# Kernel optimization log

Hardware: AMD Instinct MI355X
Metric: run time of the kernel (lower is better)

## Reference

```python
import jax, jax.numpy as jnp
import numpy as np

N_LAYERS = 6
D_MODEL = 272          # num_variables
D_STATE = 64           # d_state
D_INNER = 2 * D_MODEL  # expand=2 -> 544
D_CONV = 4
DT_RANK = 17           # ceil(272/16)
N_SCORES = 4
B, L = 4, 2048


def setup_inputs():
    key = jax.random.key(0)
    ks = jax.random.split(key, 10)
    def rn(k, shape, s=0.02):
        return jax.random.normal(k, shape, dtype=jnp.float32) * s
    A_init = jnp.broadcast_to(jnp.arange(1, D_STATE + 1, dtype=jnp.float32), (N_LAYERS, D_INNER, D_STATE))
    return {
        "x": jax.random.normal(ks[0], (B, L, D_MODEL), dtype=jnp.float32),
        "ln_w": jnp.ones((N_LAYERS, D_MODEL), jnp.float32),
        "ln_b": jnp.zeros((N_LAYERS, D_MODEL), jnp.float32),
        "in_proj_w": rn(ks[1], (N_LAYERS, 2 * D_INNER, D_MODEL)),
        "conv_w": rn(ks[2], (N_LAYERS, D_INNER, D_CONV), 0.2),
        "conv_b": jnp.zeros((N_LAYERS, D_INNER), jnp.float32),
        "x_proj_w": rn(ks[3], (N_LAYERS, DT_RANK + 2 * D_STATE, D_INNER)),
        "dt_proj_w": rn(ks[4], (N_LAYERS, D_INNER, DT_RANK), 0.1),
        "dt_proj_b": rn(ks[5], (N_LAYERS, D_INNER), 0.5),
        "A_log": jnp.log(A_init),
        "Dskip": jnp.ones((N_LAYERS, D_INNER), jnp.float32),
        "out_proj_w": rn(ks[6], (N_LAYERS, D_MODEL, D_INNER)),
        "reg_w": rn(ks[7], (N_SCORES, D_MODEL)),
        "reg_b": jnp.zeros((N_SCORES,), jnp.float32),
    }


def _layernorm(x, w, b, eps=1e-5):
    mu = x.mean(-1, keepdims=True)
    var = ((x - mu) ** 2).mean(-1, keepdims=True)
    return (x - mu) * jax.lax.rsqrt(var + eps) * w + b


def _selective_scan(u, delta, A, Bm, C, Dd):
    # u, delta: (b,l,d); Bm, C: (b,l,n); A: (d,n); Dd: (d,)
    def step(h, inp):
        d_t, B_t, C_t, u_t = inp                           # (b,d),(b,n),(b,n),(b,d)
        dA = jnp.exp(d_t[:, :, None] * A)                  # (b,d,n)
        h = dA * h + (d_t * u_t)[:, :, None] * B_t[:, None, :]
        return h, jnp.einsum('bdn,bn->bd', h, C_t)
    h0 = jnp.zeros((u.shape[0], A.shape[0], A.shape[1]), u.dtype)
    xs = tuple(jnp.swapaxes(a, 0, 1) for a in (delta, Bm, C, u))  # time-major
    _, ys = jax.lax.scan(step, h0, xs)
    return jnp.swapaxes(ys, 0, 1) + u * Dd


def _mamba_block(x, ln_w, ln_b, Wi, cw, cb, Wx, Wdt, bdt, A_log, Dd, Wo):
    h = _layernorm(x, ln_w, ln_b)
    xi, z = jnp.split(h @ Wi.T, 2, axis=-1)                # (b,l,d_inner) each
    xp = jnp.pad(xi, ((0, 0), (D_CONV - 1, 0), (0, 0)))    # causal depthwise conv
    xc = sum(xp[:, k:k + xi.shape[1], :] * cw[:, k] for k in range(D_CONV)) + cb
    xc = jax.nn.silu(xc)
    dbl = xc @ Wx.T                                        # (b,l,dt_rank+2n)
    dt, Bm, C = jnp.split(dbl, [DT_RANK, DT_RANK + D_STATE], axis=-1)
    delta = jax.nn.softplus(dt @ Wdt.T + bdt)
    y = _selective_scan(xc, delta, -jnp.exp(A_log), Bm, C, Dd)
    y = y * jax.nn.silu(z)
    return x + y @ Wo.T                                    # residual


def reference(x, ln_w, ln_b, in_proj_w, conv_w, conv_b, x_proj_w, dt_proj_w, dt_proj_b, A_log, Dskip, out_proj_w, reg_w, reg_b):
    for i in range(N_LAYERS):
        x = _mamba_block(x, ln_w[i], ln_b[i], in_proj_w[i], conv_w[i], conv_b[i],
                         x_proj_w[i], dt_proj_w[i], dt_proj_b[i], A_log[i], Dskip[i], out_proj_w[i])
    feat = x.mean(axis=1)                                  # (b, d_model)
    scores = feat @ reg_w.T + reg_b                        # (b, n_scores)
    return (scores, feat)
```

## Files before the change

kernel.cpp:

```cpp
#include <hip/hip_runtime.h>
#include <hip/hip_bf16.h>
#include <math.h>

#define NL 6
#define DM 272
#define DS 64
#define DI 544
#define DTR 17
#define NSC 4
#define BB 4
#define LL 2048
#define MTOK (BB*LL)
#define TCH 128
#define CH  16
#define DQ  (DI/4)

typedef __attribute__((ext_vector_type(8))) short bf16x8;
typedef __attribute__((ext_vector_type(4))) float f32x4;

__device__ __forceinline__ float sigmoidf_(float x){ return 1.0f/(1.0f+__expf(-x)); }
__device__ __forceinline__ unsigned short f2bfu(float x){
    union { __hip_bfloat16 h; unsigned short u; } c; c.h = __float2bfloat16(x); return c.u;
}
__device__ __forceinline__ float exp2x(float x){ float r; asm("v_exp_f32 %0, %1" : "=v"(r) : "v"(x)); return r; }

#define DPPADD(x, ctrl) x += __int_as_float(__builtin_amdgcn_update_dpp(0, __float_as_int(x), ctrl, 0xf, 0xf, true))
__device__ __forceinline__ float wsum64(float x){
    DPPADD(x, 0x111); DPPADD(x, 0x112); DPPADD(x, 0x114); DPPADD(x, 0x118);
    DPPADD(x, 0x142); DPPADD(x, 0x143);
    return x;
}

__global__ __launch_bounds__(256) void ln_kernel(const float* __restrict__ X,
                          const float* __restrict__ w,
                          const float* __restrict__ b,
                          unsigned short* __restrict__ Hb)
{
    int wave = threadIdx.x >> 6;
    int lane = threadIdx.x & 63;
    int tok = blockIdx.x*4 + wave;
    const float* xr = X + (size_t)tok*DM;
    float v[5];
    float s=0.f, ss=0.f;
    #pragma unroll
    for (int j=0;j<5;++j){
        int idx = lane + j*64;
        float x = (idx < DM) ? xr[idx] : 0.f;
        v[j]=x; s+=x; ss+=x*x;
    }
    #pragma unroll
    for (int off=1; off<64; off<<=1){ s += __shfl_xor(s,off); ss += __shfl_xor(ss,off); }
    float mu  = s * (1.0f/DM);
    float var = ss*(1.0f/DM) - mu*mu;
    float inv = 1.0f/sqrtf(var + 1e-5f);
    unsigned short* hr = Hb + (size_t)tok*DM;
    #pragma unroll
    for (int j=0;j<5;++j){
        int idx = lane + j*64;
        if (idx<DM) hr[idx] = f2bfu((v[j]-mu)*inv*w[idx] + b[idx]);
    }
}

template<bool RESID>
__global__ __launch_bounds__(256) void gmfma(const unsigned short* __restrict__ A, int lda,
                     const unsigned short* __restrict__ W, int ldw,
                     float* __restrict__ C, int ldc,
                     const float* __restrict__ R, int ldr,
                     int N, int K)
{
    __shared__ unsigned short As[128*40];
    __shared__ unsigned short Bs[128*40];
    int bm = blockIdx.x*128, bn = blockIdx.y*128;
    int tid = threadIdx.x;
    int lane = tid & 63, wave = tid >> 6;
    int wm = wave >> 1, wn = wave & 1;
    f32x4 acc[4][4] = {};
    int r16 = lane & 15, kg = (lane >> 4) * 8;
    for (int k0=0; k0<K; k0+=32){
        #pragma unroll
        for (int it=0; it<2; ++it){
            int cid = tid + it*256;
            int row = cid >> 2, kq = (cid & 3)*8;
            int kk = k0 + kq;
            uint4 za = make_uint4(0,0,0,0);
            if (kk < K) za = *(const uint4*)(A + (size_t)(bm+row)*lda + kk);
            *(uint4*)&As[row*40 + kq] = za;
            uint4 zb = make_uint4(0,0,0,0);
            int wr = bn + row;
            if (wr < N && kk < K) zb = *(const uint4*)(W + (size_t)wr*ldw + kk);
            *(uint4*)&Bs[row*40 + kq] = zb;
        }
        __syncthreads();
        bf16x8 af[4], bfr[4];
        #pragma unroll
        for (int mi=0; mi<4; ++mi)
            af[mi] = *(bf16x8*)&As[(wm*64 + mi*16 + r16)*40 + kg];
        #pragma unroll
        for (int ni=0; ni<4; ++ni)
            bfr[ni] = *(bf16x8*)&Bs[(wn*64 + ni*16 + r16)*40 + kg];
        #pragma unroll
        for (int mi=0; mi<4; ++mi)
            #pragma unroll
            for (int ni=0; ni<4; ++ni)
                acc[mi][ni] = __builtin_amdgcn_mfma_f32_16x16x32_bf16(af[mi], bfr[ni], acc[mi][ni], 0, 0, 0);
        __syncthreads();
    }
    int rowt = (lane >> 4)*4, colt = lane & 15;
    #pragma unroll
    for (int mi=0; mi<4; ++mi){
        #pragma unroll
        for (int ni=0; ni<4; ++ni){
            int col = bn + wn*64 + ni*16 + colt;
            if (col < N){
                #pragma unroll
                for (int j=0; j<4; ++j){
                    int row = bm + wm*64 + mi*16 + rowt + j;
                    float v = acc[mi][ni][j];
                    if (RESID) v += R[(size_t)row*ldr + col];
                    C[(size_t)row*ldc + col] = v;
                }
            }
        }
    }
}

__global__ __launch_bounds__(256) void conv_t2_kernel(const float* __restrict__ XZ,
                                 const float* __restrict__ cw,
                                 const float* __restrict__ cb,
                                 float* __restrict__ XCt,
                                 float* __restrict__ Gt,
                                 unsigned short* __restrict__ XCb)
{
    __shared__ float xi[67][69];
    __shared__ float zz[64][69];
    int bid = blockIdx.x;
    int b  = bid >> 8;
    int rem = bid & 255;
    int t0 = (rem >> 3)*64;
    int d0 = (rem & 7)*68;
    int tid = threadIdx.x;
    for (int li = tid; li < 67*17; li += 256){
        int row = li / 17, q = li - row*17;
        int tg = t0 - 3 + row;
        float4 v = make_float4(0.f,0.f,0.f,0.f);
        if (tg >= 0)
            v = *(const float4*)(XZ + ((size_t)b*LL + tg)*(2*DI) + d0 + q*4);
        xi[row][q*4+0]=v.x; xi[row][q*4+1]=v.y; xi[row][q*4+2]=v.z; xi[row][q*4+3]=v.w;
    }
    for (int li = tid; li < 64*17; li += 256){
        int row = li / 17, q = li - row*17;
        float4 v = *(const float4*)(XZ + ((size_t)b*LL + t0 + row)*(2*DI) + DI + d0 + q*4);
        zz[row][q*4+0]=v.x; zz[row][q*4+1]=v.y; zz[row][q*4+2]=v.z; zz[row][q*4+3]=v.w;
    }
    __syncthreads();
    int t = tid & 63;
    int dw = tid >> 6;
    float xcreg[17];
    #pragma unroll
    for (int i=0; i<17; ++i){
        int dl = dw + i*4;
        int d = d0 + dl;
        const float* cwd = cw + d*4;
        float acc = cb[d];
        #pragma unroll
        for (int k=0;k<4;++k) acc = fmaf(xi[t+k][dl], cwd[k], acc);
        float xc = acc * sigmoidf_(acc);
        float z  = zz[t][dl];
        size_t o = ((size_t)b*DI + d)*LL + t0 + t;
        XCt[o] = xc;
        Gt[o]  = z * sigmoidf_(z);
        xcreg[i] = xc;
    }
    __syncthreads();
    #pragma unroll
    for (int i=0; i<17; ++i) zz[t][dw + i*4] = xcreg[i];
    __syncthreads();
    for (int li = tid; li < 64*17; li += 256){
        int row = li / 17, q = li - row*17;
        ushort4 v;
        v.x = f2bfu(zz[row][q*4+0]); v.y = f2bfu(zz[row][q*4+1]);
        v.z = f2bfu(zz[row][q*4+2]); v.w = f2bfu(zz[row][q*4+3]);
        *(ushort4*)&XCb[((size_t)b*LL + t0 + row)*DI + d0 + q*4] = v;
    }
}

__global__ __launch_bounds__(256) void dt_t2_kernel(const float* __restrict__ DBLb,
                          const float* __restrict__ Wdt,
                          const float* __restrict__ bdt,
                          float* __restrict__ DELt)
{
    __shared__ float dtv[64*19];
    __shared__ float wl[68*17];
    int bid = blockIdx.x;
    int b  = bid >> 8;
    int rem = bid & 255;
    int t0 = (rem >> 3)*64;
    int d0 = (rem & 7)*68;
    int tid = threadIdx.x;
    for (int li = tid; li < 64*17; li += 256){
        int row = li / 17, col = li - row*17;
        dtv[row*19 + col] = DBLb[((size_t)b*LL + t0 + row)*145 + col];
    }
    for (int li = tid; li < 68*17; li += 256)
        wl[li] = Wdt[(size_t)d0*17 + li];
    __syncthreads();
    int t = tid & 63;
    #pragma unroll 1
    for (int dl = tid >> 6; dl < 68; dl += 4){
        float s = bdt[d0 + dl];
        #pragma unroll
        for (int r=0;r<DTR;++r) s = fmaf(dtv[t*19 + r], wl[dl*17 + r], s);
        float sp = (s > 20.f) ? s : log1pf(__expf(s));
        DELt[((size_t)b*DI + d0 + dl)*LL + t0 + t] = sp;
    }
}

__global__ __launch_bounds__(256) void scan_a(const float* __restrict__ DELt,
                       const float* __restrict__ XCt,
                       const float* __restrict__ DBLb,
                       const float* __restrict__ A_log,
                       float* __restrict__ Q,
                       float* __restrict__ S)
{
    __shared__ float2 dlb[4][4][64];
    int wave = threadIdx.x >> 6, lane = threadIdx.x & 63;
    float2 (*Db)[64] = dlb[wave];
    int wid = blockIdx.x*4 + wave;
    int dd = wid % DQ;
    int c  = (wid / DQ) % CH;
    int b  = wid / (DQ*CH);
    int d0 = dd, d1 = dd+DQ, d2 = dd+2*DQ, d3 = dd+3*DQ;
    const float L2E = 1.44269504f;
    float Av0 = -__expf(A_log[d0*DS + lane]) * L2E;
    float Av1 = -__expf(A_log[d1*DS + lane]) * L2E;
    float Av2 = -__expf(A_log[d2*DS + lane]) * L2E;
    float Av3 = -__expf(A_log[d3*DS + lane]) * L2E;
    float h0=0.f,h1=0.f,h2=0.f,h3=0.f, ds0=0.f,ds1=0.f,ds2=0.f,ds3=0.f;
    size_t rb0 = ((size_t)b*DI + d0)*LL + c*TCH;
    size_t rb1 = ((size_t)b*DI + d1)*LL + c*TCH;
    size_t rb2 = ((size_t)b*DI + d2)*LL + c*TCH;
    size_t rb3 = ((size_t)b*DI + d3)*LL + c*TCH;
    const float* pB = DBLb + ((size_t)b*LL + c*TCH)*145;
    for (int blk=0; blk<TCH/64; ++blk){
        size_t o0 = rb0 + blk*64 + lane, o1 = rb1 + blk*64 + lane;
        size_t o2 = rb2 + blk*64 + lane, o3 = rb3 + blk*64 + lane;
        float dl0 = DELt[o0], dl1 = DELt[o1], dl2 = DELt[o2], dl3 = DELt[o3];
        float du0 = dl0*XCt[o0], du1 = dl1*XCt[o1], du2 = dl2*XCt[o2], du3 = dl3*XCt[o3];
        ds0 += dl0; ds1 += dl1; ds2 += dl2; ds3 += dl3;
        Db[0][lane] = make_float2(dl0, du0);
        Db[1][lane] = make_float2(dl1, du1);
        Db[2][lane] = make_float2(dl2, du2);
        Db[3][lane] = make_float2(dl3, du3);
        const float* p = pB + (size_t)blk*64*145;
        #pragma unroll 1
        for (int g=0; g<8; ++g){
            const float2* q0 = &Db[0][g*8];
            const float2* q1 = &Db[1][g*8];
            const float2* q2 = &Db[2][g*8];
            const float2* q3 = &Db[3][g*8];
            #pragma unroll
            for (int i=0; i<8; ++i){
                float Bv = p[17+lane];
                float2 a0=q0[i], a1=q1[i], a2=q2[i], a3=q3[i];
                h0 = fmaf(exp2x(a0.x*Av0), h0, a0.y*Bv);
                h1 = fmaf(exp2x(a1.x*Av1), h1, a1.y*Bv);
                h2 = fmaf(exp2x(a2.x*Av2), h2, a2.y*Bv);
                h3 = fmaf(exp2x(a3.x*Av3), h3, a3.y*Bv);
                p += 145;
            }
        }
    }
    size_t q0i = ((size_t)b*DI + d0)*CH + c, q1i = ((size_t)b*DI + d1)*CH + c;
    size_t q2i = ((size_t)b*DI + d2)*CH + c, q3i = ((size_t)b*DI + d3)*CH + c;
    Q[q0i*64 + lane] = h0; Q[q1i*64 + lane] = h1;
    Q[q2i*64 + lane] = h2; Q[q3i*64 + lane] = h3;
    float s0 = wsum64(ds0), s1 = wsum64(ds1), s2 = wsum64(ds2), s3 = wsum64(ds3);
    if (lane == 63){ S[q0i]=s0; S[q1i]=s1; S[q2i]=s2; S[q3i]=s3; }
}

__global__ __launch_bounds__(256) void scan_c(const float* __restrict__ DELt,
                       float* __restrict__ XCt,
                       const float* __restrict__ Gt,
                       const float* __restrict__ DBLb,
                       const float* __restrict__ A_log,
                       const float* __restrict__ Dskip,
                       const float* __restrict__ Q,
                       const float* __restrict__ S)
{
    __shared__ float P[4][2][4][76];
    __shared__ float Ypark[4][2][4];
    __shared__ float2 dlb[4][2][64];
    int wave = threadIdx.x >> 6, lane = threadIdx.x & 63;
    float (*Pr0)[76] = P[wave][0];
    float (*Pr1)[76] = P[wave][1];
    float* Yp0 = Ypark[wave][0];
    float* Yp1 = Ypark[wave][1];
    float2* Db0 = dlb[wave][0];
    float2* Db1 = dlb[wave][1];
    int wid = blockIdx.x*4 + wave;
    int dd = wid % (DI/2);
    int c  = (wid / (DI/2)) % CH;
    int b  = wid / ((DI/2)*CH);
    int d0 = dd, d1 = dd + DI/2;
    const float L2E = 1.44269504f;
    float Av0 = -__expf(A_log[d0*DS + lane]) * L2E;
    float Av1 = -__expf(A_log[d1*DS + lane]) * L2E;
    float Dd0 = Dskip[d0], Dd1 = Dskip[d1];
    size_t q0 = ((size_t)b*DI + d0)*CH, q1 = ((size_t)b*DI + d1)*CH;
    float h0=0.f, h1=0.f;
    for (int j=0; j<c; ++j){
        h0 = fmaf(exp2x(Av0*S[q0+j]), h0, Q[(q0+j)*64 + lane]);
        h1 = fmaf(exp2x(Av1*S[q1+j]), h1, Q[(q1+j)*64 + lane]);
    }
    size_t rb0 = ((size_t)b*DI + d0)*LL + c*TCH;
    size_t rb1 = ((size_t)b*DI + d1)*LL + c*TCH;
    const float* pB = DBLb + ((size_t)b*LL + c*TCH)*145;
    int fr = lane >> 4, fq = (lane & 15)*4;
    for (int blk=0; blk<TCH/64; ++blk){
        size_t o0 = rb0 + blk*64 + lane, o1 = rb1 + blk*64 + lane;
        float dl0 = DELt[o0], dl1 = DELt[o1];
        float ul0 = XCt[o0],  ul1 = XCt[o1];
        float gl0 = Gt[o0],   gl1 = Gt[o1];
        Db0[lane] = make_float2(dl0, dl0*ul0);
        Db1[lane] = make_float2(dl1, dl1*ul1);
        float y0=0.f, y1=0.f;
        const float* p = pB + (size_t)blk*64*145;
        #pragma unroll 1
        for (int f=0; f<16; ++f){
            const float2* db0 = &Db0[f*4];
            const float2* db1 = &Db1[f*4];
            #pragma unroll
            for (int i=0; i<4; ++i){
                float Bv = p[17+lane];
                float Cv = p[81+lane];
                float2 a0 = db0[i], a1 = db1[i];
                h0 = fmaf(exp2x(a0.x*Av0), h0, a0.y*Bv);
                h1 = fmaf(exp2x(a1.x*Av1), h1, a1.y*Bv);
                Pr0[i][lane] = h0*Cv;
                Pr1[i][lane] = h1*Cv;
                p += 145;
            }
            float4 xa0 = *(const float4*)&Pr0[fr][fq];
            float s0 = (xa0.x+xa0.y)+(xa0.z+xa0.w);
            DPPADD(s0,0x111); DPPADD(s0,0x112); DPPADD(s0,0x114); DPPADD(s0,0x118);
            float4 xa1 = *(const float4*)&Pr1[fr][fq];
            float s1 = (xa1.x+xa1.y)+(xa1.z+xa1.w);
            DPPADD(s1,0x111); DPPADD(s1,0x112); DPPADD(s1,0x114); DPPADD(s1,0x118);
            if ((lane & 15) == 15){ Yp0[fr] = s0; Yp1[fr] = s1; }
            float g0 = Yp0[lane & 3];
            float g1 = Yp1[lane & 3];
            if ((lane >> 2) == f){ y0 = g0; y1 = g1; }
        }
        XCt[o0] = (y0 + ul0*Dd0)*gl0;
        XCt[o1] = (y1 + ul1*Dd1)*gl1;
    }
}

__global__ __launch_bounds__(256) void yt2yb_kernel(const float* __restrict__ Yt,
                             unsigned short* __restrict__ Yb)
{
    __shared__ float yt[64][69];
    int bid = blockIdx.x;
    int b = bid >> 8;
    int rem = bid & 255;
    int d0 = (rem >> 5)*68;
    int t0 = (rem & 31)*64;
    int tid = threadIdx.x;
    for (int li = tid; li < 68*16; li += 256){
        int dl = li >> 4, tq = (li & 15)*4;
        float4 v = *(const float4*)(Yt + ((size_t)b*DI + d0 + dl)*LL + t0 + tq);
        yt[tq+0][dl]=v.x; yt[tq+1][dl]=v.y; yt[tq+2][dl]=v.z; yt[tq+3][dl]=v.w;
    }
    __syncthreads();
    for (int li = tid; li < 64*17; li += 256){
        int row = li / 17, q = li - row*17;
        ushort4 v;
        v.x = f2bfu(yt[row][q*4+0]); v.y = f2bfu(yt[row][q*4+1]);
        v.z = f2bfu(yt[row][q*4+2]); v.w = f2bfu(yt[row][q*4+3]);
        *(ushort4*)&Yb[((size_t)b*LL + t0 + row)*DI + d0 + q*4] = v;
    }
}

__global__ __launch_bounds__(256) void wconv_kernel(const float* __restrict__ src,
                            unsigned short* __restrict__ dst,
                            int total, int kin, int kout)
{
    int idx = blockIdx.x*256 + threadIdx.x;
    if (idx >= total) return;
    int r = idx / kout, c = idx - r*kout;
    float v = (c < kin) ? src[(size_t)r*kin + c] : 0.f;
    dst[idx] = f2bfu(v);
}

__global__ __launch_bounds__(256) void head1_kernel(const float* __restrict__ X,
                             float* __restrict__ Pt)
{
    int b = blockIdx.x >> 6, c = blockIdx.x & 63;
    int tid = threadIdx.x;
    for (int dm = tid; dm < DM; dm += 256){
        float s = 0.f;
        const float* base = X + ((size_t)b*LL + c*32)*DM + dm;
        #pragma unroll 8
        for (int tt=0; tt<32; ++tt) s += base[(size_t)tt*DM];
        Pt[(size_t)(b*64 + c)*DM + dm] = s;
    }
}

__global__ __launch_bounds__(256) void head2_kernel(const float* __restrict__ Pt,
                             const float* __restrict__ reg_w,
                             const float* __restrict__ reg_b,
                             float* __restrict__ out)
{
    __shared__ float feat[DM];
    int b = blockIdx.x, tid = threadIdx.x;
    for (int dm = tid; dm < DM; dm += 256){
        float s = 0.f;
        for (int c=0; c<64; ++c) s += Pt[(size_t)(b*64 + c)*DM + dm];
        float f = s * (1.0f/LL);
        feat[dm] = f;
        out[16 + b*DM + dm] = f;
    }
    __syncthreads();
    if (tid < NSC){
        float s = reg_b[tid];
        const float* wr = reg_w + tid*DM;
        for (int k=0;k<DM;++k) s = fmaf(feat[k], wr[k], s);
        out[b*NSC + tid] = s;
    }
}

extern "C" void kernel_launch(void* const* d_in, const int* in_sizes, int n_in,
                              void* d_out, int out_size, void* d_ws, size_t ws_size,
                              hipStream_t stream)
{
    const float* x_in  = (const float*)d_in[0];
    const float* ln_w  = (const float*)d_in[1];
    const float* ln_b  = (const float*)d_in[2];
    const float* Wi    = (const float*)d_in[3];
    const float* cw    = (const float*)d_in[4];
    const float* cb    = (const float*)d_in[5];
    const float* Wx    = (const float*)d_in[6];
    const float* Wdt   = (const float*)d_in[7];
    const float* bdt   = (const float*)d_in[8];
    const float* A_log = (const float*)d_in[9];
    const float* Dd    = (const float*)d_in[10];
    const float* Wo    = (const float*)d_in[11];
    const float* regw  = (const float*)d_in[12];
    const float* regb  = (const float*)d_in[13];
    float* out = (float*)d_out;

    float* ws   = (float*)d_ws;
    float* XZ   = ws;
    float* XCt  = XZ   + (size_t)MTOK*1088;
    float* Gt   = XCt  + (size_t)MTOK*544;
    float* DBLb = Gt   + (size_t)MTOK*544;
    float* Xb   = DBLb + (size_t)MTOK*145;
    float* SCR  = Xb   + (size_t)MTOK*272;
    float* Sbuf = SCR  + (size_t)MTOK*272;
    unsigned short* WiB = (unsigned short*)(Sbuf + BB*DI*CH);
    unsigned short* WxB = WiB + (size_t)NL*1088*DM;
    unsigned short* WoB = WxB + (size_t)NL*145*DI;

    float* DELt = XZ;
    unsigned short* Yb = (unsigned short*)(XZ + (size_t)MTOK*544);
    unsigned short* Hb  = (unsigned short*)SCR;
    unsigned short* XCb = (unsigned short*)SCR;
    float* Q  = SCR;
    float* Pt = SCR;

    (void)hipMemcpyAsync(Xb, x_in, sizeof(float)*(size_t)MTOK*DM, hipMemcpyDeviceToDevice, stream);

    wconv_kernel<<<(NL*1088*DM + 255)/256, 256, 0, stream>>>(Wi, WiB, NL*1088*DM, DM, DM);
    wconv_kernel<<<(NL*145*DI + 255)/256, 256, 0, stream>>>(Wx, WxB, NL*145*DI, DI, DI);
    wconv_kernel<<<(NL*272*DI + 255)/256, 256, 0, stream>>>(Wo, WoB, NL*272*DI, DI, DI);

    for (int l=0; l<NL; ++l){
        ln_kernel<<<MTOK/4, 256, 0, stream>>>(Xb, ln_w + l*DM, ln_b + l*DM, Hb);
        gmfma<false><<<dim3(MTOK/128, (2*DI+127)/128), 256, 0, stream>>>(
            Hb, DM, WiB + (size_t)l*2*DI*DM, DM, XZ, 2*DI, nullptr, 0, 2*DI, DM);
        conv_t2_kernel<<<BB*256, 256, 0, stream>>>(XZ, cw + l*DI*4, cb + l*DI, XCt, Gt, XCb);
        gmfma<false><<<dim3(MTOK/128, 2), 256, 0, stream>>>(
            XCb, DI, WxB + (size_t)l*145*DI, DI, DBLb, 145, nullptr, 0, 145, DI);
        dt_t2_kernel<<<BB*256, 256, 0, stream>>>(DBLb, Wdt + (size_t)l*DI*DTR, bdt + l*DI, DELt);
        scan_a<<<(BB*CH*DQ)/4, 256, 0, stream>>>(DELt, XCt, DBLb,
                                                 A_log + (size_t)l*DI*DS, Q, Sbuf);
        scan_c<<<(BB*CH*(DI/2))/4, 256, 0, stream>>>(DELt, XCt, Gt, DBLb,
                                                     A_log + (size_t)l*DI*DS, Dd + l*DI, Q, Sbuf);
        yt2yb_kernel<<<BB*256, 256, 0, stream>>>(XCt, Yb);
        gmfma<true><<<dim3(MTOK/128, 3), 256, 0, stream>>>(
            Yb, DI, WoB + (size_t)l*DM*DI, DI, Xb, DM, Xb, DM, DM, DI);
    }
    head1_kernel<<<BB*64, 256, 0, stream>>>(Xb, Pt);
    head2_kernel<<<BB, 256, 0, stream>>>(Pt, regw, regb, out);
}
```

Measured before the change: 1.572 ms.

## Store XZ, conv outputs and gate in bf16; fuse Y transpose into scan_c

The in-projection GEMM now writes bf16 instead of fp32. The conv kernel reads that bf16 input and writes the transposed conv output and SiLU gate as bf16, and both scan kernels read these bf16 buffers. scan_c writes the gated output directly into the token-major bf16 Yb buffer, which removes the separate yt2yb transpose kernel. Together these halve traffic on several large intermediates and save one launch per layer, at the cost of bf16 rounding on the scan inputs and strided 2-byte scattered stores from scan_c.

```diff
diff --git a/kernel.cpp b/kernel.cpp
--- a/kernel.cpp
+++ b/kernel.cpp
@@ -22,6 +22,7 @@
 __device__ __forceinline__ unsigned short f2bfu(float x){
     union { __hip_bfloat16 h; unsigned short u; } c; c.h = __float2bfloat16(x); return c.u;
 }
+__device__ __forceinline__ float bfu2f(unsigned short u){ return __uint_as_float(((unsigned)u)<<16); }
 __device__ __forceinline__ float exp2x(float x){ float r; asm("v_exp_f32 %0, %1" : "=v"(r) : "v"(x)); return r; }
 
 #define DPPADD(x, ctrl) x += __int_as_float(__builtin_amdgcn_update_dpp(0, __float_as_int(x), ctrl, 0xf, 0xf, true))
@@ -61,10 +62,10 @@
     }
 }
 
-template<bool RESID>
+template<bool RESID, bool OUTBF16>
 __global__ __launch_bounds__(256) void gmfma(const unsigned short* __restrict__ A, int lda,
                      const unsigned short* __restrict__ W, int ldw,
-                     float* __restrict__ C, int ldc,
+                     void* __restrict__ Cv, int ldc,
                      const float* __restrict__ R, int ldr,
                      int N, int K)
 {
@@ -117,18 +118,21 @@
                     int row = bm + wm*64 + mi*16 + rowt + j;
                     float v = acc[mi][ni][j];
                     if (RESID) v += R[(size_t)row*ldr + col];
-                    C[(size_t)row*ldc + col] = v;
+                    if (OUTBF16)
+                        ((unsigned short*)Cv)[(size_t)row*ldc + col] = f2bfu(v);
+                    else
+                        ((float*)Cv)[(size_t)row*ldc + col] = v;
                 }
             }
         }
     }
 }
 
-__global__ __launch_bounds__(256) void conv_t2_kernel(const float* __restrict__ XZ,
+__global__ __launch_bounds__(256) void conv_t2_kernel(const unsigned short* __restrict__ XZb,
                                  const float* __restrict__ cw,
                                  const float* __restrict__ cb,
-                                 float* __restrict__ XCt,
-                                 float* __restrict__ Gt,
+                                 unsigned short* __restrict__ XCtb,
+                                 unsigned short* __restrict__ Gtb,
                                  unsigned short* __restrict__ XCb)
 {
     __shared__ float xi[67][69];
@@ -143,14 +147,17 @@
         int row = li / 17, q = li - row*17;
         int tg = t0 - 3 + row;
         float4 v = make_float4(0.f,0.f,0.f,0.f);
-        if (tg >= 0)
-            v = *(const float4*)(XZ + ((size_t)b*LL + tg)*(2*DI) + d0 + q*4);
+        if (tg >= 0){
+            ushort4 u4 = *(const ushort4*)(XZb + ((size_t)b*LL + tg)*(2*DI) + d0 + q*4);
+            v.x = bfu2f(u4.x); v.y = bfu2f(u4.y); v.z = bfu2f(u4.z); v.w = bfu2f(u4.w);
+        }
         xi[row][q*4+0]=v.x; xi[row][q*4+1]=v.y; xi[row][q*4+2]=v.z; xi[row][q*4+3]=v.w;
     }
     for (int li = tid; li < 64*17; li += 256){
         int row = li / 17, q = li - row*17;
-        float4 v = *(const float4*)(XZ + ((size_t)b*LL + t0 + row)*(2*DI) + DI + d0 + q*4);
-        zz[row][q*4+0]=v.x; zz[row][q*4+1]=v.y; zz[row][q*4+2]=v.z; zz[row][q*4+3]=v.w;
+        ushort4 u4 = *(const ushort4*)(XZb + ((size_t)b*LL + t0 + row)*(2*DI) + DI + d0 + q*4);
+        zz[row][q*4+0]=bfu2f(u4.x); zz[row][q*4+1]=bfu2f(u4.y);
+        zz[row][q*4+2]=bfu2f(u4.z); zz[row][q*4+3]=bfu2f(u4.w);
     }
     __syncthreads();
     int t = tid & 63;
@@ -167,8 +174,8 @@
         float xc = acc * sigmoidf_(acc);
         float z  = zz[t][dl];
         size_t o = ((size_t)b*DI + d)*LL + t0 + t;
-        XCt[o] = xc;
-        Gt[o]  = z * sigmoidf_(z);
+        XCtb[o] = f2bfu(xc);
+        Gtb[o]  = f2bfu(z * sigmoidf_(z));
         xcreg[i] = xc;
     }
     __syncthreads();
@@ -216,7 +223,7 @@
 }
 
 __global__ __launch_bounds__(256) void scan_a(const float* __restrict__ DELt,
-                       const float* __restrict__ XCt,
+                       const unsigned short* __restrict__ XCtb,
                        const float* __restrict__ DBLb,
                        const float* __restrict__ A_log,
                        float* __restrict__ Q,
@@ -245,7 +252,8 @@
         size_t o0 = rb0 + blk*64 + lane, o1 = rb1 + blk*64 + lane;
         size_t o2 = rb2 + blk*64 + lane, o3 = rb3 + blk*64 + lane;
         float dl0 = DELt[o0], dl1 = DELt[o1], dl2 = DELt[o2], dl3 = DELt[o3];
-        float du0 = dl0*XCt[o0], du1 = dl1*XCt[o1], du2 = dl2*XCt[o2], du3 = dl3*XCt[o3];
+        float du0 = dl0*bfu2f(XCtb[o0]), du1 = dl1*bfu2f(XCtb[o1]);
+        float du2 = dl2*bfu2f(XCtb[o2]), du3 = dl3*bfu2f(XCtb[o3]);
         ds0 += dl0; ds1 += dl1; ds2 += dl2; ds3 += dl3;
         Db[0][lane] = make_float2(dl0, du0);
         Db[1][lane] = make_float2(dl1, du1);
@@ -279,13 +287,14 @@
 }
 
 __global__ __launch_bounds__(256) void scan_c(const float* __restrict__ DELt,
-                       float* __restrict__ XCt,
-                       const float* __restrict__ Gt,
+                       const unsigned short* __restrict__ XCtb,
+                       const unsigned short* __restrict__ Gtb,
                        const float* __restrict__ DBLb,
                        const float* __restrict__ A_log,
                        const float* __restrict__ Dskip,
                        const float* __restrict__ Q,
-                       const float* __restrict__ S)
+                       const float* __restrict__ S,
+                       unsigned short* __restrict__ Yb)
 {
     __shared__ float P[4][2][4][76];
     __shared__ float Ypark[4][2][4];
@@ -319,8 +328,8 @@
     for (int blk=0; blk<TCH/64; ++blk){
         size_t o0 = rb0 + blk*64 + lane, o1 = rb1 + blk*64 + lane;
         float dl0 = DELt[o0], dl1 = DELt[o1];
-        float ul0 = XCt[o0],  ul1 = XCt[o1];
-        float gl0 = Gt[o0],   gl1 = Gt[o1];
+        float ul0 = bfu2f(XCtb[o0]), ul1 = bfu2f(XCtb[o1]);
+        float gl0 = bfu2f(Gtb[o0]),  gl1 = bfu2f(Gtb[o1]);
         Db0[lane] = make_float2(dl0, dl0*ul0);
         Db1[lane] = make_float2(dl1, dl1*ul1);
         float y0=0.f, y1=0.f;
@@ -351,33 +360,9 @@
             float g1 = Yp1[lane & 3];
             if ((lane >> 2) == f){ y0 = g0; y1 = g1; }
         }
-        XCt[o0] = (y0 + ul0*Dd0)*gl0;
-        XCt[o1] = (y1 + ul1*Dd1)*gl1;
-    }
-}
-
-__global__ __launch_bounds__(256) void yt2yb_kernel(const float* __restrict__ Yt,
-                             unsigned short* __restrict__ Yb)
-{
-    __shared__ float yt[64][69];
-    int bid = blockIdx.x;
-    int b = bid >> 8;
-    int rem = bid & 255;
-    int d0 = (rem >> 5)*68;
-    int t0 = (rem & 31)*64;
-    int tid = threadIdx.x;
-    for (int li = tid; li < 68*16; li += 256){
-        int dl = li >> 4, tq = (li & 15)*4;
-        float4 v = *(const float4*)(Yt + ((size_t)b*DI + d0 + dl)*LL + t0 + tq);
-        yt[tq+0][dl]=v.x; yt[tq+1][dl]=v.y; yt[tq+2][dl]=v.z; yt[tq+3][dl]=v.w;
-    }
-    __syncthreads();
-    for (int li = tid; li < 64*17; li += 256){
-        int row = li / 17, q = li - row*17;
-        ushort4 v;
-        v.x = f2bfu(yt[row][q*4+0]); v.y = f2bfu(yt[row][q*4+1]);
-        v.z = f2bfu(yt[row][q*4+2]); v.w = f2bfu(yt[row][q*4+3]);
-        *(ushort4*)&Yb[((size_t)b*LL + t0 + row)*DI + d0 + q*4] = v;
+        size_t trow = (size_t)b*LL + c*TCH + blk*64 + lane;
+        Yb[trow*DI + d0] = f2bfu((y0 + ul0*Dd0)*gl0);
+        Yb[trow*DI + d1] = f2bfu((y1 + ul1*Dd1)*gl1);
     }
 }
 
@@ -449,24 +434,27 @@
     const float* regb  = (const float*)d_in[13];
     float* out = (float*)d_out;
 
-    float* ws   = (float*)d_ws;
-    float* XZ   = ws;
-    float* XCt  = XZ   + (size_t)MTOK*1088;
-    float* Gt   = XCt  + (size_t)MTOK*544;
-    float* DBLb = Gt   + (size_t)MTOK*544;
-    float* Xb   = DBLb + (size_t)MTOK*145;
-    float* SCR  = Xb   + (size_t)MTOK*272;
-    float* Sbuf = SCR  + (size_t)MTOK*272;
-    unsigned short* WiB = (unsigned short*)(Sbuf + BB*DI*CH);
-    unsigned short* WxB = WiB + (size_t)NL*1088*DM;
-    unsigned short* WoB = WxB + (size_t)NL*145*DI;
-
-    float* DELt = XZ;
-    unsigned short* Yb = (unsigned short*)(XZ + (size_t)MTOK*544);
+    char* base = (char*)d_ws;
+    auto carve = [&](size_t bytes) -> char* {
+        char* p = base; base += (bytes + 255) & ~(size_t)255; return p;
+    };
+    unsigned short* XZb  = (unsigned short*)carve((size_t)MTOK*1088*2);
+    unsigned short* XCtb = (unsigned short*)carve((size_t)MTOK*544*2);
+    unsigned short* Gtb  = (unsigned short*)carve((size_t)MTOK*544*2);
+    float*          DELt = (float*)carve((size_t)MTOK*544*4);
+    float*          DBLb = (float*)carve((size_t)MTOK*145*4);
+    float*          Xb   = (float*)carve((size_t)MTOK*272*4);
+    unsigned short* Yb   = (unsigned short*)carve((size_t)MTOK*544*2);
+    char*           SCR  = carve((size_t)MTOK*272*4);
+    float*          Sbuf = (float*)carve((size_t)BB*DI*CH*4);
+    unsigned short* WiB  = (unsigned short*)carve((size_t)NL*1088*DM*2);
+    unsigned short* WxB  = (unsigned short*)carve((size_t)NL*145*DI*2);
+    unsigned short* WoB  = (unsigned short*)carve((size_t)NL*272*DI*2);
+
     unsigned short* Hb  = (unsigned short*)SCR;
     unsigned short* XCb = (unsigned short*)SCR;
-    float* Q  = SCR;
-    float* Pt = SCR;
+    float*          Q   = (float*)SCR;
+    float*          Pt  = (float*)SCR;
 
     (void)hipMemcpyAsync(Xb, x_in, sizeof(float)*(size_t)MTOK*DM, hipMemcpyDeviceToDevice, stream);
 
@@ -476,18 +464,17 @@
 
     for (int l=0; l<NL; ++l){
         ln_kernel<<<MTOK/4, 256, 0, stream>>>(Xb, ln_w + l*DM, ln_b + l*DM, Hb);
-        gmfma<false><<<dim3(MTOK/128, (2*DI+127)/128), 256, 0, stream>>>(
-            Hb, DM, WiB + (size_t)l*2*DI*DM, DM, XZ, 2*DI, nullptr, 0, 2*DI, DM);
-        conv_t2_kernel<<<BB*256, 256, 0, stream>>>(XZ, cw + l*DI*4, cb + l*DI, XCt, Gt, XCb);
-        gmfma<false><<<dim3(MTOK/128, 2), 256, 0, stream>>>(
+        gmfma<false,true><<<dim3(MTOK/128, (2*DI+127)/128), 256, 0, stream>>>(
+            Hb, DM, WiB + (size_t)l*2*DI*DM, DM, XZb, 2*DI, nullptr, 0, 2*DI, DM);
+        conv_t2_kernel<<<BB*256, 256, 0, stream>>>(XZb, cw + l*DI*4, cb + l*DI, XCtb, Gtb, XCb);
+        gmfma<false,false><<<dim3(MTOK/128, 2), 256, 0, stream>>>(
             XCb, DI, WxB + (size_t)l*145*DI, DI, DBLb, 145, nullptr, 0, 145, DI);
         dt_t2_kernel<<<BB*256, 256, 0, stream>>>(DBLb, Wdt + (size_t)l*DI*DTR, bdt + l*DI, DELt);
-        scan_a<<<(BB*CH*DQ)/4, 256, 0, stream>>>(DELt, XCt, DBLb,
+        scan_a<<<(BB*CH*DQ)/4, 256, 0, stream>>>(DELt, XCtb, DBLb,
                                                  A_log + (size_t)l*DI*DS, Q, Sbuf);
-        scan_c<<<(BB*CH*(DI/2))/4, 256, 0, stream>>>(DELt, XCt, Gt, DBLb,
-                                                     A_log + (size_t)l*DI*DS, Dd + l*DI, Q, Sbuf);
-        yt2yb_kernel<<<BB*256, 256, 0, stream>>>(XCt, Yb);
-        gmfma<true><<<dim3(MTOK/128, 3), 256, 0, stream>>>(
+        scan_c<<<(BB*CH*(DI/2))/4, 256, 0, stream>>>(DELt, XCtb, Gtb, DBLb,
+                                                     A_log + (size_t)l*DI*DS, Dd + l*DI, Q, Sbuf, Yb);
+        gmfma<true,false><<<dim3(MTOK/128, 3), 256, 0, stream>>>(
             Yb, DI, WoB + (size_t)l*DM*DI, DI, Xb, DM, Xb, DM, DM, DI);
     }
     head1_kernel<<<BB*64, 256, 0, stream>>>(Xb, Pt);
```

After: 1.543 ms. About the same (-1.8%).
